# Performance work log

Measured on AMD Instinct MI355X. Metric: run time of the kernel, lower is better.

The kernel has to match this reference:

```python
import jax, jax.numpy as jnp
import numpy as np

B, H, W, C = 4, 64, 64, 256
CQ = C // 8


def setup_inputs() -> dict:
    key = jax.random.key(0)
    ks = jax.random.split(key, 5)
    scale = 0.02
    inputs = jax.random.normal(ks[0], (B, H, W, C), dtype=jnp.float32)
    wq = jax.random.normal(ks[1], (C, CQ), dtype=jnp.float32) * scale
    bq = jnp.zeros((CQ,), dtype=jnp.float32)
    wk = jax.random.normal(ks[2], (C, CQ), dtype=jnp.float32) * scale
    bk = jnp.zeros((CQ,), dtype=jnp.float32)
    wv = jax.random.normal(ks[3], (C, C), dtype=jnp.float32) * scale
    bv = jnp.zeros((C,), dtype=jnp.float32)
    gamma = jax.random.normal(ks[4], (), dtype=jnp.float32)
    return {"inputs": inputs, "wq": wq, "bq": bq, "wk": wk, "bk": bk,
            "wv": wv, "bv": bv, "gamma": gamma}


def reference(inputs, wq, bq, wk, bk, wv, bv, gamma):
    b, h, w, c = inputs.shape
    n = h * w
    x = inputs.reshape(b, n, c)  # [B, N, C]
    # 1x1 convs == per-pixel linear projections
    q = x @ wq + bq              # [B, N, Cq]
    k = x @ wk + bk              # [B, N, Cq]
    v = x @ wv + bv              # [B, N, C]
    # energy = Q K^T (no sqrt scaling, as in the original)
    energy = jnp.einsum('bnd,bmd->bnm', q, k)      # [B, N, N]
    attention = jax.nn.softmax(energy, axis=-1)    # softmax over keys
    # x_out = V^T @ attention^T -> per query: sum_m attn[n,m] * v[m]
    x_out = jnp.einsum('bnm,bmc->bnc', attention, v)  # [B, N, C]
    x_out = x_out.reshape(b, h, w, c)
    return gamma * x_out + inputs
```

## Files before the change

### kernel.cpp

```cpp
#include <hip/hip_runtime.h>
#include <hip/hip_bf16.h>

typedef __attribute__((ext_vector_type(8))) short bf16x8;
typedef __attribute__((ext_vector_type(4))) float f32x4;
typedef __attribute__((ext_vector_type(16))) float f32x16;
typedef __attribute__((ext_vector_type(4))) int int4v;

#define NB 4
#define NN 4096
#define NC 256
#define NSPLIT 4
#define KEYS_PER_SPLIT 1024
#define KT_ITERS 16
#define LOG2E 1.4426950408889634f

__device__ __forceinline__ unsigned short f2bf(float f) {
    unsigned u = __builtin_bit_cast(unsigned, f);
    u += 0x7fffu + ((u >> 16) & 1u);
    return (unsigned short)(u >> 16);
}
__device__ __forceinline__ float bf2f(unsigned short u) {
    unsigned v = ((unsigned)u) << 16;
    return __builtin_bit_cast(float, v);
}
__device__ __forceinline__ void load_lds16(const void* g, void* l) {
    __builtin_amdgcn_global_load_lds(
        (const __attribute__((address_space(1))) void*)g,
        (__attribute__((address_space(3))) void*)l, 16, 0, 0);
}
__device__ __forceinline__ unsigned cvtpk(float lo, float hi) {
    unsigned d;
    asm("v_cvt_pk_bf16_f32 %0, %1, %2" : "=v"(d) : "v"(lo), "v"(hi));
    return d;
}
__device__ __forceinline__ void pl32swap(unsigned &a, unsigned &b) {
    asm volatile("v_permlane32_swap_b32 %0, %1" : "+v"(a), "+v"(b));
}
__device__ __forceinline__ float fexp2(float x) {
    float r;
    asm("v_exp_f32 %0, %1" : "=v"(r) : "v"(x));
    return r;
}
__device__ __forceinline__ float frcp(float x) {
    float r;
    asm("v_rcp_f32 %0, %1" : "=v"(r) : "v"(x));
    return r;
}

__global__ __launch_bounds__(256) void wt_kernel(
    const float* __restrict__ wq, const float* __restrict__ wk,
    const float* __restrict__ wv, unsigned short* __restrict__ wt)
{
    const int c = blockIdx.x;
    const int k = threadIdx.x;
    float v;
    if (c < 32)      v = wq[k * 32 + c];
    else if (c < 64) v = wk[k * 32 + (c - 32)] * LOG2E;
    else             v = wv[k * 256 + (c - 64)];
    wt[c * 256 + k] = f2bf(v);
}

__global__ __launch_bounds__(256) void proj_kernel(
    const float* __restrict__ x,
    const unsigned short* __restrict__ wt,
    const float* __restrict__ bq, const float* __restrict__ bk,
    const float* __restrict__ bv,
    unsigned short* __restrict__ q_ws,
    unsigned short* __restrict__ k_ws,
    unsigned short* __restrict__ vt_ws)
{
    const int lane = threadIdx.x & 63;
    const int w    = threadIdx.x >> 6;
    const int l15  = lane & 15, hh = lane >> 4;
    const int m0   = blockIdx.x * 16;
    const int ct0  = w * 5;

    f32x4 acc[5];
    #pragma unroll
    for (int i = 0; i < 5; ++i) acc[i] = f32x4{0.f, 0.f, 0.f, 0.f};

    const float* xrow = x + (size_t)(m0 + l15) * 256 + hh * 8;
    #pragma unroll
    for (int ks = 0; ks < 8; ++ks) {
        float4 xa = ((const float4*)(xrow + ks * 32))[0];
        float4 xb = ((const float4*)(xrow + ks * 32))[1];
        bf16x8 afrag;
        afrag[0] = (short)f2bf(xa.x); afrag[1] = (short)f2bf(xa.y);
        afrag[2] = (short)f2bf(xa.z); afrag[3] = (short)f2bf(xa.w);
        afrag[4] = (short)f2bf(xb.x); afrag[5] = (short)f2bf(xb.y);
        afrag[6] = (short)f2bf(xb.z); afrag[7] = (short)f2bf(xb.w);
        #pragma unroll
        for (int c = 0; c < 5; ++c) {
            bf16x8 bfrag = *(const bf16x8*)(wt + (size_t)((ct0 + c) * 16 + l15) * 256 + ks * 32 + hh * 8);
            acc[c] = __builtin_amdgcn_mfma_f32_16x16x32_bf16(afrag, bfrag, acc[c], 0, 0, 0);
        }
    }

    const int b    = m0 >> 12;
    const int nloc = m0 & 4095;
    #pragma unroll
    for (int c = 0; c < 5; ++c) {
        const int ct = ct0 + c;
        const int c0 = ct * 16;
        float bias;
        if (c0 < 32)      bias = bq[c0 + l15];
        else if (c0 < 64) bias = bk[c0 - 32 + l15] * LOG2E;
        else              bias = bv[c0 - 64 + l15];
        if (c0 < 64) {
            unsigned short* dst = (c0 < 32) ? q_ws : k_ws;
            const int cc = (c0 < 32) ? c0 : (c0 - 32);
            #pragma unroll
            for (int i = 0; i < 4; ++i)
                dst[(size_t)(m0 + hh * 4 + i) * 32 + cc + l15] = f2bf(acc[c][i] + bias);
        } else {
            const int cc = c0 - 64 + l15;
            #pragma unroll
            for (int i = 0; i < 4; i += 2) {
                unsigned lo = f2bf(acc[c][i]     + bias);
                unsigned hi = f2bf(acc[c][i + 1] + bias);
                *(unsigned*)(vt_ws + ((size_t)b * 256 + cc) * 4096 + nloc + hh * 4 + i)
                    = lo | (hi << 16);
            }
        }
    }
}

__global__ __launch_bounds__(512, 4) void attn_kernel(
    const unsigned short* __restrict__ q_ws,
    const unsigned short* __restrict__ k_ws,
    const unsigned short* __restrict__ vt_ws,
    unsigned short* __restrict__ opart,
    float* __restrict__ lpart)
{
    __shared__ unsigned short vt_lds[2 * 256 * 64];

    const int lane = threadIdx.x & 63;
    const int wid  = threadIdx.x >> 6;
    const int l31  = lane & 31;
    const int hi   = lane >> 5;
    const int wr   = wid >> 1;
    const int wc   = wid & 1;

    const int xcd   = blockIdx.x & 7;
    const int j     = blockIdx.x >> 3;
    const int combo = xcd * 2 + (j >> 5);
    const int qtile = j & 31;
    const int split = combo >> 2;
    const int b     = combo & 3;
    const int q0    = qtile * 128;
    const int key0  = split * KEYS_PER_SPLIT;

    bf16x8 aq[2];
    #pragma unroll
    for (int cs = 0; cs < 2; ++cs)
        aq[cs] = *(const bf16x8*)(q_ws +
            (size_t)(b * 4096 + q0 + wr * 32 + l31) * 32 + cs * 16 + hi * 8);

    f32x16 acc[4];
    #pragma unroll
    for (int ct = 0; ct < 4; ++ct)
        #pragma unroll
        for (int r = 0; r < 16; ++r) acc[ct][r] = 0.f;
    float lsum = 0.f;

    const unsigned short* vt_base = vt_ws + (size_t)b * 256 * 4096;
    const unsigned short* k_base  = k_ws + (size_t)b * 4096 * 32;

    #pragma unroll
    for (int e = 0; e < 4; ++e) {
        int idx  = e * 512 + threadIdx.x;
        int c    = idx >> 3;
        int slot = idx & 7;
        const unsigned short* src = vt_base + (size_t)c * 4096 + key0 + ((slot ^ (c & 7)) << 3);
        load_lds16(src, (char*)vt_lds + idx * 16);
    }

    for (int kt = 0; kt < KT_ITERS; ++kt) {
        const int kb      = key0 + kt * 64;
        const int cur_off = (kt & 1) << 15;

        __syncthreads();

        if (kt + 1 < KT_ITERS) {
            const int nxt_off = cur_off ^ 32768;
            #pragma unroll
            for (int e = 0; e < 4; ++e) {
                int idx  = e * 512 + threadIdx.x;
                int c    = idx >> 3;
                int slot = idx & 7;
                const unsigned short* src = vt_base + (size_t)c * 4096 + (kb + 64) + ((slot ^ (c & 7)) << 3);
                load_lds16(src, (char*)vt_lds + nxt_off + idx * 16);
            }
        }

        unsigned pa[4][4];
        #pragma unroll
        for (int ktile = 0; ktile < 2; ++ktile) {
            bf16x8 ak0 = *(const bf16x8*)(k_base +
                (size_t)(kb + ktile * 32 + l31) * 32 + hi * 8);
            bf16x8 ak1 = *(const bf16x8*)(k_base +
                (size_t)(kb + ktile * 32 + l31) * 32 + 16 + hi * 8);
            f32x16 e0;
            #pragma unroll
            for (int r = 0; r < 16; ++r) e0[r] = 0.f;
            e0 = __builtin_amdgcn_mfma_f32_32x32x16_bf16(ak0, aq[0], e0, 0, 0, 0);
            e0 = __builtin_amdgcn_mfma_f32_32x32x16_bf16(ak1, aq[1], e0, 0, 0, 0);

            float s = 0.f;
            #pragma unroll
            for (int h = 0; h < 2; ++h) {
                float p0 = fexp2(e0[h*8+0]), p1 = fexp2(e0[h*8+1]);
                float p2 = fexp2(e0[h*8+2]), p3 = fexp2(e0[h*8+3]);
                float p4 = fexp2(e0[h*8+4]), p5 = fexp2(e0[h*8+5]);
                float p6 = fexp2(e0[h*8+6]), p7 = fexp2(e0[h*8+7]);
                s += ((p0 + p1) + (p2 + p3)) + ((p4 + p5) + (p6 + p7));
                unsigned d0 = cvtpk(p0, p1);
                unsigned d1 = cvtpk(p2, p3);
                unsigned d2 = cvtpk(p4, p5);
                unsigned d3 = cvtpk(p6, p7);
                pl32swap(d0, d2);
                pl32swap(d1, d3);
                const int ks = ktile * 2 + h;
                pa[ks][0] = d0; pa[ks][1] = d1;
                pa[ks][2] = d2; pa[ks][3] = d3;
            }
            lsum += s;
        }

        __builtin_amdgcn_s_setprio(1);
        #pragma unroll
        for (int ks = 0; ks < 4; ++ks) {
            union { unsigned u[4]; bf16x8 v; } cvt;
            cvt.u[0] = pa[ks][0]; cvt.u[1] = pa[ks][1];
            cvt.u[2] = pa[ks][2]; cvt.u[3] = pa[ks][3];
            #pragma unroll
            for (int ct = 0; ct < 4; ++ct) {
                int c = wc * 128 + ct * 32 + l31;
                int chunk = ks * 2 + hi;
                bf16x8 bvf = *(const bf16x8*)((char*)vt_lds + cur_off + c * 128 + ((chunk ^ (c & 7)) << 4));
                acc[ct] = __builtin_amdgcn_mfma_f32_32x32x16_bf16(cvt.v, bvf, acc[ct], 0, 0, 0);
            }
        }
        __builtin_amdgcn_s_setprio(0);
    }

    lsum += __shfl_xor(lsum, 32);

    const size_t rowb = (size_t)(split * 4 + b) * 4096 + q0 + wr * 32;
    if (wc == 0 && hi == 0)
        lpart[rowb + l31] = lsum;

    #pragma unroll
    for (int ct = 0; ct < 4; ++ct) {
        int col = wc * 128 + ct * 32 + l31;
        #pragma unroll
        for (int rr = 0; rr < 16; ++rr) {
            int row = (rr & 3) + 8 * (rr >> 2) + 4 * hi;
            opart[(rowb + row) * 256 + col] = f2bf(acc[ct][rr]);
        }
    }
}

__global__ __launch_bounds__(256) void combine_kernel(
    const unsigned short* __restrict__ opart,
    const float* __restrict__ lpart,
    const float* __restrict__ x,
    const float* __restrict__ gamma_p,
    float* __restrict__ out)
{
    const int t  = blockIdx.x * 256 + threadIdx.x;
    const int r  = t >> 5;
    const int c0 = (t & 31) * 8;
    const float gamma = gamma_p[0];

    float suml = (lpart[r] + lpart[16384 + r]) +
                 (lpart[2 * 16384 + r] + lpart[3 * 16384 + r]);
    const float inv = gamma * frcp(suml);

    float sumO[8];
    #pragma unroll
    for (int j = 0; j < 8; ++j) sumO[j] = 0.f;
    #pragma unroll
    for (int s = 0; s < NSPLIT; ++s) {
        bf16x8 o = *(const bf16x8*)(opart + ((size_t)(s * 16384 + r)) * 256 + c0);
        #pragma unroll
        for (int j = 0; j < 8; ++j) sumO[j] += bf2f((unsigned short)o[j]);
    }
    const size_t base = (size_t)r * 256 + c0;
    float4 x0 = *(const float4*)(x + base);
    float4 x1 = *(const float4*)(x + base + 4);
    float4 o0, o1;
    o0.x = sumO[0] * inv + x0.x; o0.y = sumO[1] * inv + x0.y;
    o0.z = sumO[2] * inv + x0.z; o0.w = sumO[3] * inv + x0.w;
    o1.x = sumO[4] * inv + x1.x; o1.y = sumO[5] * inv + x1.y;
    o1.z = sumO[6] * inv + x1.z; o1.w = sumO[7] * inv + x1.w;
    *(float4*)(out + base)     = o0;
    *(float4*)(out + base + 4) = o1;
}

extern "C" void kernel_launch(void* const* d_in, const int* in_sizes, int n_in,
                              void* d_out, int out_size, void* d_ws, size_t ws_size,
                              hipStream_t stream) {
    const float* x     = (const float*)d_in[0];
    const float* wq    = (const float*)d_in[1];
    const float* bq    = (const float*)d_in[2];
    const float* wk    = (const float*)d_in[3];
    const float* bk    = (const float*)d_in[4];
    const float* wv    = (const float*)d_in[5];
    const float* bv    = (const float*)d_in[6];
    const float* gamma = (const float*)d_in[7];
    float* out = (float*)d_out;

    char* ws = (char*)d_ws;
    unsigned short* wt    = (unsigned short*)(ws);
    unsigned short* q_ws  = (unsigned short*)(ws + 163840);
    unsigned short* k_ws  = (unsigned short*)(ws + 1212416);
    unsigned short* vt_ws = (unsigned short*)(ws + 2260992);
    unsigned short* opart = (unsigned short*)(ws + 10649600);
    float*          lpart = (float*)(ws + 44204032);

    wt_kernel     <<<320,  256, 0, stream>>>(wq, wk, wv, wt);
    proj_kernel   <<<1024, 256, 0, stream>>>(x, wt, bq, bk, bv, q_ws, k_ws, vt_ws);
    attn_kernel   <<<512,  512, 0, stream>>>(q_ws, k_ws, vt_ws, opart, lpart);
    combine_kernel<<<2048, 256, 0, stream>>>(opart, lpart, x, gamma, out);
}
```

Measured before the change: 103.2 us.

## Fuse split-K combine into attention kernel via last-block atomic counter

Removes the separate combine kernel. Each attention block now bumps a per-(batch, query-tile) atomic counter after writing its partial output and row sums, and the last of the four split blocks reduces all partials, normalizes, adds gamma-scaled output to the residual and writes the result. Counters are zeroed in the weight-transpose kernel. This saves one kernel launch and lets the combine overlap with other attention blocks, at the cost of fences, an atomic, and a serialized tail on the last-arriving block.

```diff
diff --git a/kernel.cpp b/kernel.cpp
--- a/kernel.cpp
+++ b/kernel.cpp
@@ -49,10 +49,12 @@
 
 __global__ __launch_bounds__(256) void wt_kernel(
     const float* __restrict__ wq, const float* __restrict__ wk,
-    const float* __restrict__ wv, unsigned short* __restrict__ wt)
+    const float* __restrict__ wv, unsigned short* __restrict__ wt,
+    int* __restrict__ counters)
 {
     const int c = blockIdx.x;
     const int k = threadIdx.x;
+    if (c == 0 && k < 128) counters[k] = 0;
     float v;
     if (c < 32)      v = wq[k * 32 + c];
     else if (c < 64) v = wk[k * 32 + (c - 32)] * LOG2E;
@@ -130,12 +132,18 @@
     const unsigned short* __restrict__ k_ws,
     const unsigned short* __restrict__ vt_ws,
     unsigned short* __restrict__ opart,
-    float* __restrict__ lpart)
+    float* __restrict__ lpart,
+    const float* __restrict__ x,
+    const float* __restrict__ gamma_p,
+    float* __restrict__ out,
+    int* __restrict__ counters)
 {
     __shared__ unsigned short vt_lds[2 * 256 * 64];
-
-    const int lane = threadIdx.x & 63;
-    const int wid  = threadIdx.x >> 6;
+    __shared__ int lastflag;
+
+    const int tid  = threadIdx.x;
+    const int lane = tid & 63;
+    const int wid  = tid >> 6;
     const int l31  = lane & 31;
     const int hi   = lane >> 5;
     const int wr   = wid >> 1;
@@ -168,7 +176,7 @@
 
     #pragma unroll
     for (int e = 0; e < 4; ++e) {
-        int idx  = e * 512 + threadIdx.x;
+        int idx  = e * 512 + tid;
         int c    = idx >> 3;
         int slot = idx & 7;
         const unsigned short* src = vt_base + (size_t)c * 4096 + key0 + ((slot ^ (c & 7)) << 3);
@@ -185,7 +193,7 @@
             const int nxt_off = cur_off ^ 32768;
             #pragma unroll
             for (int e = 0; e < 4; ++e) {
-                int idx  = e * 512 + threadIdx.x;
+                int idx  = e * 512 + tid;
                 int c    = idx >> 3;
                 int slot = idx & 7;
                 const unsigned short* src = vt_base + (size_t)c * 4096 + (kb + 64) + ((slot ^ (c & 7)) << 3);
@@ -259,43 +267,46 @@
             opart[(rowb + row) * 256 + col] = f2bf(acc[ct][rr]);
         }
     }
-}
-
-__global__ __launch_bounds__(256) void combine_kernel(
-    const unsigned short* __restrict__ opart,
-    const float* __restrict__ lpart,
-    const float* __restrict__ x,
-    const float* __restrict__ gamma_p,
-    float* __restrict__ out)
-{
-    const int t  = blockIdx.x * 256 + threadIdx.x;
-    const int r  = t >> 5;
-    const int c0 = (t & 31) * 8;
-    const float gamma = gamma_p[0];
-
-    float suml = (lpart[r] + lpart[16384 + r]) +
-                 (lpart[2 * 16384 + r] + lpart[3 * 16384 + r]);
-    const float inv = gamma * frcp(suml);
-
-    float sumO[8];
-    #pragma unroll
-    for (int j = 0; j < 8; ++j) sumO[j] = 0.f;
-    #pragma unroll
-    for (int s = 0; s < NSPLIT; ++s) {
-        bf16x8 o = *(const bf16x8*)(opart + ((size_t)(s * 16384 + r)) * 256 + c0);
-        #pragma unroll
-        for (int j = 0; j < 8; ++j) sumO[j] += bf2f((unsigned short)o[j]);
-    }
-    const size_t base = (size_t)r * 256 + c0;
-    float4 x0 = *(const float4*)(x + base);
-    float4 x1 = *(const float4*)(x + base + 4);
-    float4 o0, o1;
-    o0.x = sumO[0] * inv + x0.x; o0.y = sumO[1] * inv + x0.y;
-    o0.z = sumO[2] * inv + x0.z; o0.w = sumO[3] * inv + x0.w;
-    o1.x = sumO[4] * inv + x1.x; o1.y = sumO[5] * inv + x1.y;
-    o1.z = sumO[6] * inv + x1.z; o1.w = sumO[7] * inv + x1.w;
-    *(float4*)(out + base)     = o0;
-    *(float4*)(out + base + 4) = o1;
+
+    __threadfence();
+    __syncthreads();
+    if (tid == 0) {
+        int old = atomicAdd(&counters[b * 32 + qtile], 1);
+        lastflag = (old == NSPLIT - 1);
+    }
+    __syncthreads();
+    if (lastflag) {
+        __threadfence();
+        const float gamma = gamma_p[0];
+        const int rr = tid >> 5;
+        const int cc = (tid & 31) * 8;
+        #pragma unroll
+        for (int it = 0; it < 8; ++it) {
+            const size_t grow = (size_t)b * 4096 + q0 + it * 16 + rr;
+            float suml = (lpart[grow] + lpart[16384 + grow]) +
+                         (lpart[2 * 16384 + grow] + lpart[3 * 16384 + grow]);
+            const float inv = gamma * frcp(suml);
+            float sumO[8];
+            #pragma unroll
+            for (int jj = 0; jj < 8; ++jj) sumO[jj] = 0.f;
+            #pragma unroll
+            for (int s = 0; s < NSPLIT; ++s) {
+                bf16x8 o = *(const bf16x8*)(opart + ((size_t)(s * 16384) + grow) * 256 + cc);
+                #pragma unroll
+                for (int jj = 0; jj < 8; ++jj) sumO[jj] += bf2f((unsigned short)o[jj]);
+            }
+            const size_t base = grow * 256 + cc;
+            float4 x0 = *(const float4*)(x + base);
+            float4 x1 = *(const float4*)(x + base + 4);
+            float4 o0, o1;
+            o0.x = sumO[0] * inv + x0.x; o0.y = sumO[1] * inv + x0.y;
+            o0.z = sumO[2] * inv + x0.z; o0.w = sumO[3] * inv + x0.w;
+            o1.x = sumO[4] * inv + x1.x; o1.y = sumO[5] * inv + x1.y;
+            o1.z = sumO[6] * inv + x1.z; o1.w = sumO[7] * inv + x1.w;
+            *(float4*)(out + base)     = o0;
+            *(float4*)(out + base + 4) = o1;
+        }
+    }
 }
 
 extern "C" void kernel_launch(void* const* d_in, const int* in_sizes, int n_in,
@@ -318,9 +329,10 @@
     unsigned short* vt_ws = (unsigned short*)(ws + 2260992);
     unsigned short* opart = (unsigned short*)(ws + 10649600);
     float*          lpart = (float*)(ws + 44204032);
-
-    wt_kernel     <<<320,  256, 0, stream>>>(wq, wk, wv, wt);
-    proj_kernel   <<<1024, 256, 0, stream>>>(x, wt, bq, bk, bv, q_ws, k_ws, vt_ws);
-    attn_kernel   <<<512,  512, 0, stream>>>(q_ws, k_ws, vt_ws, opart, lpart);
-    combine_kernel<<<2048, 256, 0, stream>>>(opart, lpart, x, gamma, out);
-}
+    int*            ctrs  = (int*)(ws + 44466176);
+
+    wt_kernel  <<<320,  256, 0, stream>>>(wq, wk, wv, wt, ctrs);
+    proj_kernel<<<1024, 256, 0, stream>>>(x, wt, bq, bk, bv, q_ws, k_ws, vt_ws);
+    attn_kernel<<<512,  512, 0, stream>>>(q_ws, k_ws, vt_ws, opart, lpart,
+                                          x, gamma, out, ctrs);
+}
```

New measurement: 307.2 us. 2.98x slower.
